# Performance work log

Measured on AMD Instinct MI355X. Metric: run time of the kernel, lower is better.

## Reference

```python
import jax, jax.numpy as jnp
import numpy as np

N = 100_000        # num nodes
F_DIM = 512        # input feature dim (num_features)
HID = 32           # hidden dim hardcoded in Encoder's GConv
E = 3_200_000      # num edges (avg degree 32)
PE1, PE2 = 0.2, 0.4   # edge removal probs
PF1, PF2 = 0.3, 0.4   # feature masking probs


def setup_inputs() -> dict:
    key = jax.random.key(0)
    ks = jax.random.split(key, 10)
    x = jax.random.normal(ks[0], (N, F_DIM), dtype=jnp.float32)
    edge_index = jax.random.randint(ks[1], (2, E), 0, N, dtype=jnp.int32).astype(jnp.int64)
    edge_weight = jnp.ones((E,), dtype=jnp.float32)
    edge_mask1 = (jax.random.uniform(ks[2], (E,)) > PE1).astype(jnp.float32)
    edge_mask2 = (jax.random.uniform(ks[3], (E,)) > PE2).astype(jnp.float32)
    feat_mask1 = (jax.random.uniform(ks[4], (F_DIM,)) > PF1).astype(jnp.float32)
    feat_mask2 = (jax.random.uniform(ks[5], (F_DIM,)) > PF2).astype(jnp.float32)
    s1 = 1.0 / np.sqrt(F_DIM)
    s2 = 1.0 / np.sqrt(HID)
    W1 = jax.random.normal(ks[6], (F_DIM, HID), dtype=jnp.float32) * s1
    b1 = jnp.zeros((HID,), dtype=jnp.float32)
    W2 = jax.random.normal(ks[7], (HID, HID), dtype=jnp.float32) * s2
    b2 = jnp.zeros((HID,), dtype=jnp.float32)
    return dict(x=x, edge_index=edge_index, edge_weight=edge_weight,
                edge_mask1=edge_mask1, edge_mask2=edge_mask2,
                feat_mask1=feat_mask1, feat_mask2=feat_mask2,
                W1=W1, b1=b1, W2=W2, b2=b2)


def _gcn_layer(h, W, b, src, dst, ew):
    # PyG GCNConv: h' = D^{-1/2} (A + I) D^{-1/2} (h W) + b, D from edge weights + self-loop
    h = h @ W                                             # [N, out]
    deg = jax.ops.segment_sum(ew, dst, num_segments=N) + 1.0   # self-loop weight 1
    dinv = jax.lax.rsqrt(deg)                             # deg >= 1, always finite
    norm = dinv[src] * ew * dinv[dst]                     # [E]
    agg = jax.ops.segment_sum(h[src] * norm[:, None], dst, num_segments=N)
    agg = agg + h * (dinv * dinv)[:, None]                # self-loop contribution
    return agg + b


def _gconv(x, edge_index, ew, W1, b1, W2, b2):
    src, dst = edge_index[0], edge_index[1]
    z = jax.nn.relu(_gcn_layer(x, W1, b1, src, dst, ew))
    z = jax.nn.relu(_gcn_layer(z, W2, b2, src, dst, ew))
    return z


def reference(x, edge_index, edge_weight, edge_mask1, edge_mask2,
              feat_mask1, feat_mask2, W1, b1, W2, b2):
    # view 0: original graph
    z = _gconv(x, edge_index, edge_weight, W1, b1, W2, b2)
    # view 1: EdgeRemoving(pe=0.2) as zeroed edge weights + FeatureMasking(pf=0.3)
    z1 = _gconv(x * feat_mask1[None, :], edge_index, edge_weight * edge_mask1, W1, b1, W2, b2)
    # view 2: EdgeRemoving(pe=0.4) + FeatureMasking(pf=0.4)
    z2 = _gconv(x * feat_mask2[None, :], edge_index, edge_weight * edge_mask2, W1, b1, W2, b2)
    return (z, z1, z2)
```

## Files before the change

### kernel.cpp

```cpp
#include <hip/hip_runtime.h>
#include <hip/hip_bf16.h>

#define F_DIMC 512
#define HIDC   32
#define NPB    4

__global__ void k_wc(const float* __restrict__ W1, const float* __restrict__ fm1,
                     const float* __restrict__ fm2, float* __restrict__ Wc) {
    int i = blockIdx.x * blockDim.x + threadIdx.x;
    if (i >= F_DIMC * HIDC) return;
    int k = i / HIDC, j = i % HIDC;
    float w = W1[i];
    float* row = Wc + k * 96;
    row[j]      = w;
    row[32 + j] = w * fm1[k];
    row[64 + j] = w * fm2[k];
}

__global__ void k_count(const int* __restrict__ dst, int* __restrict__ cnt, int E) {
    int e = blockIdx.x * blockDim.x + threadIdx.x;
    if (e >= E) return;
    atomicAdd(&cnt[dst[e]], 1);
}

__global__ void k_scan1(const int* __restrict__ cnt, int* __restrict__ off,
                        int* __restrict__ bsum, int n) {
    __shared__ int sh[256];
    int tid = threadIdx.x;
    int i0 = blockIdx.x * 1024 + tid * 4;
    int c[4]; int s = 0;
    #pragma unroll
    for (int q = 0; q < 4; q++) { int idx = i0 + q; c[q] = (idx < n) ? cnt[idx] : 0; s += c[q]; }
    sh[tid] = s; __syncthreads();
    for (int st = 1; st < 256; st <<= 1) {
        int v = (tid >= st) ? sh[tid - st] : 0;
        __syncthreads();
        sh[tid] += v;
        __syncthreads();
    }
    int incl = sh[tid];
    int ex = incl - s;
    if (tid == 255) bsum[blockIdx.x] = incl;
    int run = ex;
    #pragma unroll
    for (int q = 0; q < 4; q++) { int idx = i0 + q; if (idx <= n) off[idx] = run; run += c[q]; }
}

__global__ void k_scan2(const int* __restrict__ bsum, int* __restrict__ bex, int nb) {
    __shared__ int sh[256];
    int tid = threadIdx.x;
    int s = (tid < nb) ? bsum[tid] : 0;
    sh[tid] = s; __syncthreads();
    for (int st = 1; st < 256; st <<= 1) {
        int v = (tid >= st) ? sh[tid - st] : 0;
        __syncthreads();
        sh[tid] += v;
        __syncthreads();
    }
    if (tid < nb) bex[tid] = sh[tid] - s;
}

__global__ void k_scan3(int* __restrict__ off, int* __restrict__ cur,
                        const int* __restrict__ bex, int n) {
    int tid = threadIdx.x;
    int i0 = blockIdx.x * 1024 + tid * 4;
    int add = bex[blockIdx.x];
    #pragma unroll
    for (int q = 0; q < 4; q++) {
        int idx = i0 + q;
        if (idx <= n) {
            int v = off[idx] + add;
            off[idx] = v;
            if (idx < n) cur[idx] = v;
        }
    }
}

__global__ void k_fill(const int* __restrict__ ei, const float* __restrict__ ew,
                       const float* __restrict__ m1, const float* __restrict__ m2,
                       int* __restrict__ cur, float4* __restrict__ sorted, int E) {
    int e = blockIdx.x * blockDim.x + threadIdx.x;
    if (e >= E) return;
    int s = ei[e];
    int d = ei[E + e];
    float w = ew[e];
    int pos = atomicAdd(&cur[d], 1);
    sorted[pos] = make_float4(w, w * m1[e], w * m2[e], __int_as_float(s));
}

__global__ __launch_bounds__(256) void k_deg(const float4* __restrict__ sorted,
                                             const int* __restrict__ off,
                                             float4* __restrict__ dinv, int n) {
    int t = blockIdx.x * 256 + threadIdx.x;
    int g = t >> 2;
    int L = t & 3;
    if (g >= n) return;
    int p0 = off[g], p1 = off[g + 1];
    float sx = 0.f, sy = 0.f, sz = 0.f;
    for (int p = p0 + L; p < p1; p += 4) {
        float4 pk = sorted[p];
        sx += pk.x; sy += pk.y; sz += pk.z;
    }
    #pragma unroll
    for (int m = 1; m < 4; m <<= 1) {
        sx += __shfl_xor(sx, m);
        sy += __shfl_xor(sy, m);
        sz += __shfl_xor(sz, m);
    }
    if (L == 0)
        dinv[g] = make_float4(1.0f / sqrtf(sx + 1.0f),
                              1.0f / sqrtf(sy + 1.0f),
                              1.0f / sqrtf(sz + 1.0f), 0.0f);
}

__device__ __forceinline__ float sel3(float4 q, int v) {
    return (v == 0) ? q.x : ((v == 1) ? q.y : q.z);
}

__global__ __launch_bounds__(384) void k_agg1(const float* __restrict__ h1,
                                              const float4* __restrict__ sorted,
                                              const int* __restrict__ off,
                                              const float* __restrict__ dinvf,
                                              const float* __restrict__ b1,
                                              const float* __restrict__ W2,
                                              float* __restrict__ h2, int n) {
    __shared__ float  w2s[HIDC * HIDC];
    __shared__ float4 red[NPB][4][24];
    __shared__ float  zrow[NPB][96];
    int t = threadIdx.x;
    for (int i = t; i < HIDC * HIDC; i += 384) w2s[i] = W2[i];
    int nl = t / 96, tn = t % 96;
    int nidx = blockIdx.x * NPB + nl;
    int eg = tn / 24, c4 = tn % 24;
    int ch0 = c4 * 4;
    int v = ch0 >> 5;
    bool valid = nidx < n;
    float4 acc = make_float4(0.f, 0.f, 0.f, 0.f);
    if (valid) {
        int p0 = off[nidx], p1 = off[nidx + 1];
        int p = p0 + eg;
        for (; p + 4 < p1; p += 8) {
            float4 pk0 = sorted[p];
            float4 pk1 = sorted[p + 4];
            int s0 = __float_as_int(pk0.w);
            int s1 = __float_as_int(pk1.w);
            float nw0 = sel3(pk0, v) * dinvf[s0 * 4 + v];
            float nw1 = sel3(pk1, v) * dinvf[s1 * 4 + v];
            float4 g0 = *(const float4*)&h1[(size_t)s0 * 96 + ch0];
            float4 g1 = *(const float4*)&h1[(size_t)s1 * 96 + ch0];
            acc.x += g0.x * nw0 + g1.x * nw1;
            acc.y += g0.y * nw0 + g1.y * nw1;
            acc.z += g0.z * nw0 + g1.z * nw1;
            acc.w += g0.w * nw0 + g1.w * nw1;
        }
        if (p < p1) {
            float4 pk = sorted[p];
            int s = __float_as_int(pk.w);
            float nw = sel3(pk, v) * dinvf[s * 4 + v];
            float4 g = *(const float4*)&h1[(size_t)s * 96 + ch0];
            acc.x += g.x * nw; acc.y += g.y * nw;
            acc.z += g.z * nw; acc.w += g.w * nw;
        }
    }
    red[nl][eg][c4] = acc;
    __syncthreads();
    if (eg == 0 && valid) {
        float4 r0 = red[nl][0][c4], r1 = red[nl][1][c4];
        float4 r2 = red[nl][2][c4], r3 = red[nl][3][c4];
        float dvv = dinvf[nidx * 4 + v];
        float4 hs = *(const float4*)&h1[(size_t)nidx * 96 + ch0];
        float4 bb = *(const float4*)&b1[ch0 & 31];
        float4 z;
        z.x = fmaxf((r0.x + r1.x + r2.x + r3.x + hs.x * dvv) * dvv + bb.x, 0.f);
        z.y = fmaxf((r0.y + r1.y + r2.y + r3.y + hs.y * dvv) * dvv + bb.y, 0.f);
        z.z = fmaxf((r0.z + r1.z + r2.z + r3.z + hs.z * dvv) * dvv + bb.z, 0.f);
        z.w = fmaxf((r0.w + r1.w + r2.w + r3.w + hs.w * dvv) * dvv + bb.w, 0.f);
        *(float4*)&zrow[nl][ch0] = z;
    }
    __syncthreads();
    if (valid) {
        int j = tn & 31, v2 = tn >> 5;
        float sum = 0.f;
        #pragma unroll
        for (int k = 0; k < HIDC; k++) sum += zrow[nl][v2 * 32 + k] * w2s[k * 32 + j];
        h2[(size_t)nidx * 96 + tn] = sum;
    }
}

__global__ __launch_bounds__(384) void k_agg2(const float* __restrict__ h2,
                                              const float4* __restrict__ sorted,
                                              const int* __restrict__ off,
                                              const float* __restrict__ dinvf,
                                              const float* __restrict__ b2,
                                              float* __restrict__ out, int n) {
    __shared__ float4 red[NPB][4][24];
    int t = threadIdx.x;
    int nl = t / 96, tn = t % 96;
    int nidx = blockIdx.x * NPB + nl;
    int eg = tn / 24, c4 = tn % 24;
    int ch0 = c4 * 4;
    int v = ch0 >> 5;
    bool valid = nidx < n;
    float4 acc = make_float4(0.f, 0.f, 0.f, 0.f);
    if (valid) {
        int p0 = off[nidx], p1 = off[nidx + 1];
        int p = p0 + eg;
        for (; p + 4 < p1; p += 8) {
            float4 pk0 = sorted[p];
            float4 pk1 = sorted[p + 4];
            int s0 = __float_as_int(pk0.w);
            int s1 = __float_as_int(pk1.w);
            float nw0 = sel3(pk0, v) * dinvf[s0 * 4 + v];
            float nw1 = sel3(pk1, v) * dinvf[s1 * 4 + v];
            float4 g0 = *(const float4*)&h2[(size_t)s0 * 96 + ch0];
            float4 g1 = *(const float4*)&h2[(size_t)s1 * 96 + ch0];
            acc.x += g0.x * nw0 + g1.x * nw1;
            acc.y += g0.y * nw0 + g1.y * nw1;
            acc.z += g0.z * nw0 + g1.z * nw1;
            acc.w += g0.w * nw0 + g1.w * nw1;
        }
        if (p < p1) {
            float4 pk = sorted[p];
            int s = __float_as_int(pk.w);
            float nw = sel3(pk, v) * dinvf[s * 4 + v];
            float4 g = *(const float4*)&h2[(size_t)s * 96 + ch0];
            acc.x += g.x * nw; acc.y += g.y * nw;
            acc.z += g.z * nw; acc.w += g.w * nw;
        }
    }
    red[nl][eg][c4] = acc;
    __syncthreads();
    if (eg == 0 && valid) {
        float4 r0 = red[nl][0][c4], r1 = red[nl][1][c4];
        float4 r2 = red[nl][2][c4], r3 = red[nl][3][c4];
        float dvv = dinvf[nidx * 4 + v];
        float4 hs = *(const float4*)&h2[(size_t)nidx * 96 + ch0];
        float4 bb = *(const float4*)&b2[ch0 & 31];
        float4 z;
        z.x = fmaxf((r0.x + r1.x + r2.x + r3.x + hs.x * dvv) * dvv + bb.x, 0.f);
        z.y = fmaxf((r0.y + r1.y + r2.y + r3.y + hs.y * dvv) * dvv + bb.y, 0.f);
        z.z = fmaxf((r0.z + r1.z + r2.z + r3.z + hs.z * dvv) * dvv + bb.z, 0.f);
        z.w = fmaxf((r0.w + r1.w + r2.w + r3.w + hs.w * dvv) * dvv + bb.w, 0.f);
        *(float4*)&out[((size_t)v * n + nidx) * HIDC + (ch0 & 31)] = z;
    }
}

__global__ __launch_bounds__(192) void k_gemm1(const float* __restrict__ x,
                                               const float* __restrict__ Wc,
                                               float* __restrict__ h1, int n) {
    __shared__ float xs[32][132];
    __shared__ float wsd[32][96];
    int tid = threadIdx.x;
    int m0 = blockIdx.x * 128;
    int rg = tid & 15, cg = tid >> 4;
    float acc[8][8] = {};
    for (int kt = 0; kt < F_DIMC; kt += 32) {
        for (int i = tid; i < 1024; i += 192) {
            int r = i >> 3, kc = i & 7;
            float4 v = make_float4(0.f, 0.f, 0.f, 0.f);
            int row = m0 + r;
            if (row < n) v = *(const float4*)&x[(size_t)row * F_DIMC + kt + kc * 4];
            xs[kc * 4 + 0][r] = v.x;
            xs[kc * 4 + 1][r] = v.y;
            xs[kc * 4 + 2][r] = v.z;
            xs[kc * 4 + 3][r] = v.w;
        }
        for (int i = tid; i < 768; i += 192) {
            int k = i / 24, c4 = i % 24;
            *(float4*)&wsd[k][c4 * 4] = *(const float4*)&Wc[(size_t)(kt + k) * 96 + c4 * 4];
        }
        __syncthreads();
        #pragma unroll 4
        for (int k = 0; k < 32; k++) {
            float a[8], b[8];
            *(float4*)&a[0] = *(float4*)&xs[k][rg * 8];
            *(float4*)&a[4] = *(float4*)&xs[k][rg * 8 + 4];
            *(float4*)&b[0] = *(float4*)&wsd[k][cg * 8];
            *(float4*)&b[4] = *(float4*)&wsd[k][cg * 8 + 4];
            #pragma unroll
            for (int i = 0; i < 8; i++) {
                #pragma unroll
                for (int j = 0; j < 8; j++) acc[i][j] += a[i] * b[j];
            }
        }
        __syncthreads();
    }
    #pragma unroll
    for (int i = 0; i < 8; i++) {
        int row = m0 + rg * 8 + i;
        if (row < n) {
            float4 v0 = make_float4(acc[i][0], acc[i][1], acc[i][2], acc[i][3]);
            float4 v1 = make_float4(acc[i][4], acc[i][5], acc[i][6], acc[i][7]);
            *(float4*)&h1[(size_t)row * 96 + cg * 8]     = v0;
            *(float4*)&h1[(size_t)row * 96 + cg * 8 + 4] = v1;
        }
    }
}

extern "C" void kernel_launch(void* const* d_in, const int* in_sizes, int n_in,
                              void* d_out, int out_size, void* d_ws, size_t ws_size,
                              hipStream_t stream) {
    const float* x   = (const float*)d_in[0];
    const int*   ei  = (const int*)d_in[1];
    const float* ew  = (const float*)d_in[2];
    const float* m1  = (const float*)d_in[3];
    const float* m2  = (const float*)d_in[4];
    const float* fm1 = (const float*)d_in[5];
    const float* fm2 = (const float*)d_in[6];
    const float* W1  = (const float*)d_in[7];
    const float* b1  = (const float*)d_in[8];
    const float* W2  = (const float*)d_in[9];
    const float* b2  = (const float*)d_in[10];
    float* out = (float*)d_out;
    int Nn = in_sizes[0] / F_DIMC;
    int Ee = in_sizes[2];
    (void)n_in; (void)out_size; (void)ws_size;

    char* ws = (char*)d_ws;
    size_t o = 0;
    auto carve = [&](size_t bytes) -> char* {
        char* p = ws + o;
        o = (o + bytes + 255) & ~(size_t)255;
        return p;
    };
    int*    cnt    = (int*)   carve((size_t)Nn * 4);
    int*    off    = (int*)   carve(((size_t)Nn + 1) * 4);
    int*    bsum   = (int*)   carve(256 * 4);
    int*    bex    = (int*)   carve(256 * 4);
    float4* dinv   = (float4*)carve((size_t)Nn * 16);
    float4* sorted = (float4*)carve((size_t)Ee * 16);
    float*  h1     = (float*) carve((size_t)Nn * 96 * 4);
    float*  h2     = (float*) carve((size_t)Nn * 96 * 4);
    float*  Wc     = (float*) carve((size_t)F_DIMC * 96 * 4);

    hipMemsetAsync(cnt, 0, (size_t)Nn * 4, stream);

    k_wc<<<(F_DIMC * HIDC + 255) / 256, 256, 0, stream>>>(W1, fm1, fm2, Wc);
    k_count<<<(Ee + 255) / 256, 256, 0, stream>>>(ei + Ee, cnt, Ee);
    int nb = (Nn + 1023) / 1024;
    k_scan1<<<nb, 256, 0, stream>>>(cnt, off, bsum, Nn);
    k_scan2<<<1, 256, 0, stream>>>(bsum, bex, nb);
    k_scan3<<<nb, 256, 0, stream>>>(off, cnt, bex, Nn);
    k_fill<<<(Ee + 255) / 256, 256, 0, stream>>>(ei, ew, m1, m2, cnt, sorted, Ee);
    k_deg<<<(Nn * 4 + 255) / 256, 256, 0, stream>>>(sorted, off, dinv, Nn);
    k_gemm1<<<(Nn + 127) / 128, 192, 0, stream>>>(x, Wc, h1, Nn);
    k_agg1<<<(Nn + NPB - 1) / NPB, 384, 0, stream>>>(h1, sorted, off, (const float*)dinv,
                                                     b1, W2, h2, Nn);
    k_agg2<<<(Nn + NPB - 1) / NPB, 384, 0, stream>>>(h2, sorted, off, (const float*)dinv,
                                                     b2, out, Nn);
}
```

Measured before the change: 1.229 ms.

## Pack CSR edges into float2 with mask bits, record atomic rank, retile gemm1

The sorted edge records shrink from float4 (weight, two masked weights, src) to float2. The two edge-removal masks are stored as bits 30 and 31 of the source index, which cuts the edge-stream bandwidth in the degree and both aggregation kernels. The count kernel now stores each edge's atomic rank, so the fill pass computes its position without a second atomic. This costs an extra E-sized int buffer to write and read. The first-layer GEMM moves from 192 threads with 8x8 microtiles to 256 threads with 4x12 microtiles. The bit-packing relies on the masks being exactly 0/1 and on node ids fitting in 30 bits.

```diff
diff --git a/kernel.cpp b/kernel.cpp
--- a/kernel.cpp
+++ b/kernel.cpp
@@ -17,10 +17,11 @@
     row[64 + j] = w * fm2[k];
 }
 
-__global__ void k_count(const int* __restrict__ dst, int* __restrict__ cnt, int E) {
+__global__ void k_count(const int* __restrict__ dst, int* __restrict__ cnt,
+                        int* __restrict__ rank, int E) {
     int e = blockIdx.x * blockDim.x + threadIdx.x;
     if (e >= E) return;
-    atomicAdd(&cnt[dst[e]], 1);
+    rank[e] = atomicAdd(&cnt[dst[e]], 1);
 }
 
 __global__ void k_scan1(const int* __restrict__ cnt, int* __restrict__ off,
@@ -60,35 +61,33 @@
     if (tid < nb) bex[tid] = sh[tid] - s;
 }
 
-__global__ void k_scan3(int* __restrict__ off, int* __restrict__ cur,
-                        const int* __restrict__ bex, int n) {
+__global__ void k_scan3(int* __restrict__ off, const int* __restrict__ bex, int n) {
     int tid = threadIdx.x;
     int i0 = blockIdx.x * 1024 + tid * 4;
     int add = bex[blockIdx.x];
     #pragma unroll
     for (int q = 0; q < 4; q++) {
         int idx = i0 + q;
-        if (idx <= n) {
-            int v = off[idx] + add;
-            off[idx] = v;
-            if (idx < n) cur[idx] = v;
-        }
+        if (idx <= n) off[idx] += add;
     }
 }
 
 __global__ void k_fill(const int* __restrict__ ei, const float* __restrict__ ew,
                        const float* __restrict__ m1, const float* __restrict__ m2,
-                       int* __restrict__ cur, float4* __restrict__ sorted, int E) {
+                       const int* __restrict__ off, const int* __restrict__ rank,
+                       float2* __restrict__ sorted, int E) {
     int e = blockIdx.x * blockDim.x + threadIdx.x;
     if (e >= E) return;
     int s = ei[e];
     int d = ei[E + e];
-    float w = ew[e];
-    int pos = atomicAdd(&cur[d], 1);
-    sorted[pos] = make_float4(w, w * m1[e], w * m2[e], __int_as_float(s));
-}
-
-__global__ __launch_bounds__(256) void k_deg(const float4* __restrict__ sorted,
+    unsigned bits = (unsigned)s;
+    if (m1[e] > 0.5f) bits |= (1u << 30);
+    if (m2[e] > 0.5f) bits |= (1u << 31);
+    int pos = off[d] + rank[e];
+    sorted[pos] = make_float2(ew[e], __uint_as_float(bits));
+}
+
+__global__ __launch_bounds__(256) void k_deg(const float2* __restrict__ sorted,
                                              const int* __restrict__ off,
                                              float4* __restrict__ dinv, int n) {
     int t = blockIdx.x * 256 + threadIdx.x;
@@ -98,8 +97,11 @@
     int p0 = off[g], p1 = off[g + 1];
     float sx = 0.f, sy = 0.f, sz = 0.f;
     for (int p = p0 + L; p < p1; p += 4) {
-        float4 pk = sorted[p];
-        sx += pk.x; sy += pk.y; sz += pk.z;
+        float2 pk = sorted[p];
+        unsigned bb = __float_as_uint(pk.y);
+        sx += pk.x;
+        sy += (bb & (1u << 30)) ? pk.x : 0.f;
+        sz += (bb & (1u << 31)) ? pk.x : 0.f;
     }
     #pragma unroll
     for (int m = 1; m < 4; m <<= 1) {
@@ -113,12 +115,8 @@
                               1.0f / sqrtf(sz + 1.0f), 0.0f);
 }
 
-__device__ __forceinline__ float sel3(float4 q, int v) {
-    return (v == 0) ? q.x : ((v == 1) ? q.y : q.z);
-}
-
 __global__ __launch_bounds__(384) void k_agg1(const float* __restrict__ h1,
-                                              const float4* __restrict__ sorted,
+                                              const float2* __restrict__ sorted,
                                               const int* __restrict__ off,
                                               const float* __restrict__ dinvf,
                                               const float* __restrict__ b1,
@@ -140,12 +138,14 @@
         int p0 = off[nidx], p1 = off[nidx + 1];
         int p = p0 + eg;
         for (; p + 4 < p1; p += 8) {
-            float4 pk0 = sorted[p];
-            float4 pk1 = sorted[p + 4];
-            int s0 = __float_as_int(pk0.w);
-            int s1 = __float_as_int(pk1.w);
-            float nw0 = sel3(pk0, v) * dinvf[s0 * 4 + v];
-            float nw1 = sel3(pk1, v) * dinvf[s1 * 4 + v];
+            float2 pk0 = sorted[p];
+            float2 pk1 = sorted[p + 4];
+            unsigned q0 = __float_as_uint(pk0.y), q1 = __float_as_uint(pk1.y);
+            int s0 = q0 & 0x3FFFFFFF, s1 = q1 & 0x3FFFFFFF;
+            float k0 = (v == 0) ? 1.f : (float)((q0 >> (29 + v)) & 1u);
+            float k1 = (v == 0) ? 1.f : (float)((q1 >> (29 + v)) & 1u);
+            float nw0 = pk0.x * k0 * dinvf[s0 * 4 + v];
+            float nw1 = pk1.x * k1 * dinvf[s1 * 4 + v];
             float4 g0 = *(const float4*)&h1[(size_t)s0 * 96 + ch0];
             float4 g1 = *(const float4*)&h1[(size_t)s1 * 96 + ch0];
             acc.x += g0.x * nw0 + g1.x * nw1;
@@ -154,9 +154,11 @@
             acc.w += g0.w * nw0 + g1.w * nw1;
         }
         if (p < p1) {
-            float4 pk = sorted[p];
-            int s = __float_as_int(pk.w);
-            float nw = sel3(pk, v) * dinvf[s * 4 + v];
+            float2 pk = sorted[p];
+            unsigned q = __float_as_uint(pk.y);
+            int s = q & 0x3FFFFFFF;
+            float kk = (v == 0) ? 1.f : (float)((q >> (29 + v)) & 1u);
+            float nw = pk.x * kk * dinvf[s * 4 + v];
             float4 g = *(const float4*)&h1[(size_t)s * 96 + ch0];
             acc.x += g.x * nw; acc.y += g.y * nw;
             acc.z += g.z * nw; acc.w += g.w * nw;
@@ -188,7 +190,7 @@
 }
 
 __global__ __launch_bounds__(384) void k_agg2(const float* __restrict__ h2,
-                                              const float4* __restrict__ sorted,
+                                              const float2* __restrict__ sorted,
                                               const int* __restrict__ off,
                                               const float* __restrict__ dinvf,
                                               const float* __restrict__ b2,
@@ -206,12 +208,14 @@
         int p0 = off[nidx], p1 = off[nidx + 1];
         int p = p0 + eg;
         for (; p + 4 < p1; p += 8) {
-            float4 pk0 = sorted[p];
-            float4 pk1 = sorted[p + 4];
-            int s0 = __float_as_int(pk0.w);
-            int s1 = __float_as_int(pk1.w);
-            float nw0 = sel3(pk0, v) * dinvf[s0 * 4 + v];
-            float nw1 = sel3(pk1, v) * dinvf[s1 * 4 + v];
+            float2 pk0 = sorted[p];
+            float2 pk1 = sorted[p + 4];
+            unsigned q0 = __float_as_uint(pk0.y), q1 = __float_as_uint(pk1.y);
+            int s0 = q0 & 0x3FFFFFFF, s1 = q1 & 0x3FFFFFFF;
+            float k0 = (v == 0) ? 1.f : (float)((q0 >> (29 + v)) & 1u);
+            float k1 = (v == 0) ? 1.f : (float)((q1 >> (29 + v)) & 1u);
+            float nw0 = pk0.x * k0 * dinvf[s0 * 4 + v];
+            float nw1 = pk1.x * k1 * dinvf[s1 * 4 + v];
             float4 g0 = *(const float4*)&h2[(size_t)s0 * 96 + ch0];
             float4 g1 = *(const float4*)&h2[(size_t)s1 * 96 + ch0];
             acc.x += g0.x * nw0 + g1.x * nw1;
@@ -220,9 +224,11 @@
             acc.w += g0.w * nw0 + g1.w * nw1;
         }
         if (p < p1) {
-            float4 pk = sorted[p];
-            int s = __float_as_int(pk.w);
-            float nw = sel3(pk, v) * dinvf[s * 4 + v];
+            float2 pk = sorted[p];
+            unsigned q = __float_as_uint(pk.y);
+            int s = q & 0x3FFFFFFF;
+            float kk = (v == 0) ? 1.f : (float)((q >> (29 + v)) & 1u);
+            float nw = pk.x * kk * dinvf[s * 4 + v];
             float4 g = *(const float4*)&h2[(size_t)s * 96 + ch0];
             acc.x += g.x * nw; acc.y += g.y * nw;
             acc.z += g.z * nw; acc.w += g.w * nw;
@@ -245,17 +251,18 @@
     }
 }
 
-__global__ __launch_bounds__(192) void k_gemm1(const float* __restrict__ x,
+__global__ __launch_bounds__(256) void k_gemm1(const float* __restrict__ x,
                                                const float* __restrict__ Wc,
                                                float* __restrict__ h1, int n) {
     __shared__ float xs[32][132];
     __shared__ float wsd[32][96];
     int tid = threadIdx.x;
     int m0 = blockIdx.x * 128;
-    int rg = tid & 15, cg = tid >> 4;
-    float acc[8][8] = {};
+    int rg = tid & 31;
+    int cg = tid >> 5;
+    float acc[4][12] = {};
     for (int kt = 0; kt < F_DIMC; kt += 32) {
-        for (int i = tid; i < 1024; i += 192) {
+        for (int i = tid; i < 1024; i += 256) {
             int r = i >> 3, kc = i & 7;
             float4 v = make_float4(0.f, 0.f, 0.f, 0.f);
             int row = m0 + r;
@@ -265,34 +272,34 @@
             xs[kc * 4 + 2][r] = v.z;
             xs[kc * 4 + 3][r] = v.w;
         }
-        for (int i = tid; i < 768; i += 192) {
+        for (int i = tid; i < 768; i += 256) {
             int k = i / 24, c4 = i % 24;
             *(float4*)&wsd[k][c4 * 4] = *(const float4*)&Wc[(size_t)(kt + k) * 96 + c4 * 4];
         }
         __syncthreads();
-        #pragma unroll 4
+        #pragma unroll 8
         for (int k = 0; k < 32; k++) {
-            float a[8], b[8];
-            *(float4*)&a[0] = *(float4*)&xs[k][rg * 8];
-            *(float4*)&a[4] = *(float4*)&xs[k][rg * 8 + 4];
-            *(float4*)&b[0] = *(float4*)&wsd[k][cg * 8];
-            *(float4*)&b[4] = *(float4*)&wsd[k][cg * 8 + 4];
+            float a[4], b[12];
+            *(float4*)&a[0] = *(float4*)&xs[k][rg * 4];
+            *(float4*)&b[0] = *(float4*)&wsd[k][cg * 12];
+            *(float4*)&b[4] = *(float4*)&wsd[k][cg * 12 + 4];
+            *(float4*)&b[8] = *(float4*)&wsd[k][cg * 12 + 8];
             #pragma unroll
-            for (int i = 0; i < 8; i++) {
+            for (int i = 0; i < 4; i++) {
                 #pragma unroll
-                for (int j = 0; j < 8; j++) acc[i][j] += a[i] * b[j];
+                for (int j = 0; j < 12; j++) acc[i][j] += a[i] * b[j];
             }
         }
         __syncthreads();
     }
     #pragma unroll
-    for (int i = 0; i < 8; i++) {
-        int row = m0 + rg * 8 + i;
+    for (int i = 0; i < 4; i++) {
+        int row = m0 + rg * 4 + i;
         if (row < n) {
-            float4 v0 = make_float4(acc[i][0], acc[i][1], acc[i][2], acc[i][3]);
-            float4 v1 = make_float4(acc[i][4], acc[i][5], acc[i][6], acc[i][7]);
-            *(float4*)&h1[(size_t)row * 96 + cg * 8]     = v0;
-            *(float4*)&h1[(size_t)row * 96 + cg * 8 + 4] = v1;
+            float* dst = &h1[(size_t)row * 96 + cg * 12];
+            *(float4*)&dst[0] = make_float4(acc[i][0], acc[i][1], acc[i][2], acc[i][3]);
+            *(float4*)&dst[4] = make_float4(acc[i][4], acc[i][5], acc[i][6], acc[i][7]);
+            *(float4*)&dst[8] = make_float4(acc[i][8], acc[i][9], acc[i][10], acc[i][11]);
         }
     }
 }
@@ -327,8 +334,9 @@
     int*    off    = (int*)   carve(((size_t)Nn + 1) * 4);
     int*    bsum   = (int*)   carve(256 * 4);
     int*    bex    = (int*)   carve(256 * 4);
+    int*    rank   = (int*)   carve((size_t)Ee * 4);
     float4* dinv   = (float4*)carve((size_t)Nn * 16);
-    float4* sorted = (float4*)carve((size_t)Ee * 16);
+    float2* sorted = (float2*)carve((size_t)Ee * 8);
     float*  h1     = (float*) carve((size_t)Nn * 96 * 4);
     float*  h2     = (float*) carve((size_t)Nn * 96 * 4);
     float*  Wc     = (float*) carve((size_t)F_DIMC * 96 * 4);
@@ -336,14 +344,14 @@
     hipMemsetAsync(cnt, 0, (size_t)Nn * 4, stream);
 
     k_wc<<<(F_DIMC * HIDC + 255) / 256, 256, 0, stream>>>(W1, fm1, fm2, Wc);
-    k_count<<<(Ee + 255) / 256, 256, 0, stream>>>(ei + Ee, cnt, Ee);
+    k_count<<<(Ee + 255) / 256, 256, 0, stream>>>(ei + Ee, cnt, rank, Ee);
     int nb = (Nn + 1023) / 1024;
     k_scan1<<<nb, 256, 0, stream>>>(cnt, off, bsum, Nn);
     k_scan2<<<1, 256, 0, stream>>>(bsum, bex, nb);
-    k_scan3<<<nb, 256, 0, stream>>>(off, cnt, bex, Nn);
-    k_fill<<<(Ee + 255) / 256, 256, 0, stream>>>(ei, ew, m1, m2, cnt, sorted, Ee);
+    k_scan3<<<nb, 256, 0, stream>>>(off, bex, Nn);
+    k_fill<<<(Ee + 255) / 256, 256, 0, stream>>>(ei, ew, m1, m2, off, rank, sorted, Ee);
     k_deg<<<(Nn * 4 + 255) / 256, 256, 0, stream>>>(sorted, off, dinv, Nn);
-    k_gemm1<<<(Nn + 127) / 128, 192, 0, stream>>>(x, Wc, h1, Nn);
+    k_gemm1<<<(Nn + 127) / 128, 256, 0, stream>>>(x, Wc, h1, Nn);
     k_agg1<<<(Nn + NPB - 1) / NPB, 384, 0, stream>>>(h1, sorted, off, (const float*)dinv,
                                                      b1, W2, h2, Nn);
     k_agg2<<<(Nn + NPB - 1) / NPB, 384, 0, stream>>>(h2, sorted, off, (const float*)dinv,
```

Result: faster. 1.064 ms (-13.5%).
